# Kernel tuning notes

Hardware: AMD Instinct MI355X
Metric: run time of the kernel (lower is better)

Reference implementation:

```python
import jax, jax.numpy as jnp
import numpy as np

D = 1024  # d_model

def setup_inputs() -> dict:
    key = jax.random.key(0)
    ks = jax.random.split(key, 12)
    s = 1.0 / np.sqrt(D)  # torch Linear default init scale
    inp = {
        "q": jax.random.normal(ks[0], (4, 4096, D), dtype=jnp.float32),
        "k": jax.random.normal(ks[1], (4, 4096, D), dtype=jnp.float32),
        "v": jax.random.normal(ks[2], (4, 4096, D), dtype=jnp.float32),
        "Wq": jax.random.uniform(ks[3], (D, D), jnp.float32, -s, s),
        "bq": jax.random.uniform(ks[4], (D,), jnp.float32, -s, s),
        "Wk": jax.random.uniform(ks[5], (D, D), jnp.float32, -s, s),
        "bk": jax.random.uniform(ks[6], (D,), jnp.float32, -s, s),
        "Wv": jax.random.uniform(ks[7], (D, D), jnp.float32, -s, s),
        "bv": jax.random.uniform(ks[8], (D,), jnp.float32, -s, s),
        "Wo": jax.random.uniform(ks[9], (D, D), jnp.float32, -s, s),
        "bo": jax.random.uniform(ks[10], (D,), jnp.float32, -s, s),
    }
    return inp

def reference(q, k, v, Wq, bq, Wk, bk, Wv, bv, Wo, bo):
    # phi feature map: exp(-x^2 / 2)
    phi = lambda x: jnp.exp(-0.5 * x * x)
    Q = phi(q @ Wq.T + bq)            # [B, N, D]
    K = phi(k @ Wk.T + bk)            # [B, N, D]
    V = v @ Wv.T + bv                 # [B, N, D]
    # linear attention: aggregate K^T V once, then contract with Q
    KV = jnp.einsum('bnd,bnl->bdl', K, V)                 # [B, D, D]
    Z = 1.0 / (jnp.einsum('bnd,bd->bn', Q, K.sum(axis=1)) + 1e-6)  # [B, N]
    out = jnp.einsum('bnd,bdl->bnl', Q, KV) * Z[..., None]         # [B, N, D]
    return out @ Wo.T + bo
```

## Files before the change

kernel.cpp:

```cpp
#include <hip/hip_runtime.h>

typedef unsigned short u16;
typedef unsigned int u32;
typedef unsigned long long u64;

typedef __attribute__((ext_vector_type(8))) short short8;
typedef __attribute__((ext_vector_type(4))) float floatx4;

__device__ __forceinline__ float b2f(u16 h) {
  u32 u = ((u32)h) << 16;
  return __builtin_bit_cast(float, u);
}
__device__ __forceinline__ u16 f2b(float f) {
  u32 u = __builtin_bit_cast(u32, f);
  u32 r = 0x7FFFu + ((u >> 16) & 1u);
  return (u16)((u + r) >> 16);
}

__device__ __forceinline__ void gl_lds16(const void* g, void* l) {
  __builtin_amdgcn_global_load_lds(
      (__attribute__((address_space(1))) void*)(u64)g,
      (__attribute__((address_space(3))) void*)(u32)(u64)l, 16, 0, 0);
}

enum { EPI_PHI_BIAS = 0, EPI_BIAS = 1, EPI_NONE = 2,
       EPI_ZBIAS_F32 = 3 };

template<int EPI, bool TRANS_OUT>
__global__ __launch_bounds__(256)
void gemm_bt(const u16* __restrict__ Ap, const u16* __restrict__ Bp0,
             const float* __restrict__ bias, const float* __restrict__ Zall,
             void* __restrict__ Cp,
             int M, int N, int K, int ldA, int ldB, int ldC,
             long sAb, long sBb, long sCb, long sZb, int abmask, int kshift)
{
  constexpr int BSTRIDE = 16384;
  constexpr int BOFF    = 8192;
  constexpr int SMEM3   = 3 * BSTRIDE;
  constexpr int SMEM    = (TRANS_OUT && 34816 > SMEM3) ? 34816 : SMEM3;
  __shared__ char smem[SMEM];

  const int tid  = threadIdx.x;
  const int lane = tid & 63;
  const int wave = tid >> 6;
  const int wm = wave >> 1, wn = wave & 1;
  const int fl = lane & 15;
  const int q  = lane >> 4;
  const int r4 = q * 4;
  const int bm0 = blockIdx.x * 128, bn0 = blockIdx.y * 128;
  const int bz = blockIdx.z;
  const int abz = bz & abmask;
  const int kbase = (bz >> kshift) * K;

  const u16* Ah = Ap  + (size_t)abz * sAb + kbase;
  const u16* Bh = Bp0 + (size_t)abz * sBb + kbase;

  const u16* gA[2]; const u16* gB[2]; int sL[2];
  #pragma unroll
  for (int n = 0; n < 2; ++n) {
    int j = n * 256 + tid;
    int R = j >> 3, u = (j & 7) ^ (R & 7);
    int r = (R << 1) | (u >> 2), c = u & 3;
    gA[n] = Ah + (size_t)(bm0 + r) * ldA + c * 8;
    gB[n] = Bh + (size_t)(bn0 + r) * ldB + c * 8;
    sL[n] = (n * 256 + wave * 64) * 16;
  }

  int aoff[4], boff[4];
  #pragma unroll
  for (int i = 0; i < 4; ++i) {
    int ra = wm * 64 + i * 16 + fl;
    int Ra = ra >> 1, ua = ((((ra & 1) << 2) | q) ^ (Ra & 7));
    aoff[i] = (Ra * 8 + ua) * 16;
    int rb = wn * 64 + i * 16 + fl;
    int Rb = rb >> 1, ub = ((((rb & 1) << 2) | q) ^ (Rb & 7));
    boff[i] = (Rb * 8 + ub) * 16;
  }

  floatx4 zero = {0.f, 0.f, 0.f, 0.f};
  floatx4 acc[4][4];
  #pragma unroll
  for (int i = 0; i < 4; ++i)
    #pragma unroll
    for (int j = 0; j < 4; ++j) acc[i][j] = zero;

  auto stage = [&](int k0, char* base) {
    #pragma unroll
    for (int n = 0; n < 2; ++n) gl_lds16(gA[n] + k0, base + sL[n]);
    #pragma unroll
    for (int n = 0; n < 2; ++n) gl_lds16(gB[n] + k0, base + BOFF + sL[n]);
  };

  auto kstep = [&](const char* bufc) {
    short8 aF[4], bF[4];
    #pragma unroll
    for (int i = 0; i < 4; ++i) aF[i] = *(const short8*)(bufc + aoff[i]);
    #pragma unroll
    for (int i = 0; i < 4; ++i) bF[i] = *(const short8*)(bufc + BOFF + boff[i]);
    __builtin_amdgcn_s_setprio(1);
    #pragma unroll
    for (int mi = 0; mi < 4; ++mi)
      #pragma unroll
      for (int ni = 0; ni < 4; ++ni)
        acc[mi][ni] = __builtin_amdgcn_mfma_f32_16x16x32_bf16(
            aF[mi], bF[ni], acc[mi][ni], 0, 0, 0);
    __builtin_amdgcn_s_setprio(0);
  };

  const int NIT = K >> 5;
  stage(0, smem);
  stage(32, smem + BSTRIDE);
  asm volatile("s_waitcnt vmcnt(4)\ns_barrier" ::: "memory");
  int c0 = 0, c2 = 2 * BSTRIDE;
  for (int n = 0; n < NIT; ++n) {
    bool pf = n + 2 < NIT;
    if (pf) stage((n + 2) * 32, smem + c2);
    kstep(smem + c0);
    if (n + 1 < NIT) {
      if (pf) asm volatile("s_waitcnt vmcnt(4) lgkmcnt(0)\ns_barrier" ::: "memory");
      else    asm volatile("s_waitcnt vmcnt(0) lgkmcnt(0)\ns_barrier" ::: "memory");
    }
    c0 = c0 == 2 * BSTRIDE ? 0 : c0 + BSTRIDE;
    c2 = c2 == 2 * BSTRIDE ? 0 : c2 + BSTRIDE;
  }

  if constexpr (!TRANS_OUT) {
    #pragma unroll
    for (int mi = 0; mi < 4; ++mi) {
      #pragma unroll
      for (int ni = 0; ni < 4; ++ni) {
        int col = bn0 + wn * 64 + ni * 16 + fl;
        #pragma unroll
        for (int r = 0; r < 4; ++r) {
          int row = bm0 + wm * 64 + mi * 16 + r4 + r;
          float vv = acc[mi][ni][r];
          if constexpr (EPI == EPI_PHI_BIAS) {
            vv += bias[col];
            vv = __expf(-0.5f * vv * vv);
          }
          if constexpr (EPI == EPI_BIAS) vv += bias[col];
          if constexpr (EPI == EPI_ZBIAS_F32)
            vv = vv * Zall[(size_t)abz * sZb + row] + bias[col];
          if constexpr (EPI == EPI_ZBIAS_F32)
            ((float*)Cp)[(size_t)bz * sCb + (size_t)row * ldC + col] = vv;
          else
            ((u16*)Cp)[(size_t)bz * sCb + (size_t)row * ldC + col] = f2b(vv);
        }
      }
    }
  } else {
    __syncthreads();
    u16* sT = (u16*)smem;
    #pragma unroll
    for (int mi = 0; mi < 4; ++mi) {
      #pragma unroll
      for (int ni = 0; ni < 4; ++ni) {
        int colL = wn * 64 + ni * 16 + fl;
        int row0 = wm * 64 + mi * 16 + r4;
        float bcol = bias[bn0 + colL];
        ushort4 h;
        #pragma unroll
        for (int r = 0; r < 4; ++r) {
          float vv = acc[mi][ni][r] + bcol;
          if constexpr (EPI == EPI_PHI_BIAS) vv = __expf(-0.5f * vv * vv);
          ((u16*)&h)[r] = f2b(vv);
        }
        *(ushort4*)(sT + colL * 136 + row0) = h;
      }
    }
    __syncthreads();
    #pragma unroll
    for (int i = 0; i < 8; ++i) {
      int c = tid + i * 256;
      int dloc = c >> 4, t8 = (c & 15) * 8;
      int4 vv = *(const int4*)(sT + dloc * 136 + t8);
      int gd = bn0 + dloc;
      int gt = bm0 + t8;
      int batch = gt >> 12, tt = gt & 4095;
      *(int4*)((u16*)Cp + ((size_t)batch * N + gd) * 4096 + tt) = vv;
    }
  }
}

__global__ __launch_bounds__(256)
void fcvt(const float* __restrict__ src, u16* __restrict__ dst) {
  size_t i = ((size_t)blockIdx.x * 256 + threadIdx.x) * 8;
  float4 a = *(const float4*)(src + i);
  float4 b = *(const float4*)(src + i + 4);
  union { ushort4 h[2]; int4 v; } o;
  o.h[0].x = f2b(a.x); o.h[0].y = f2b(a.y); o.h[0].z = f2b(a.z); o.h[0].w = f2b(a.w);
  o.h[1].x = f2b(b.x); o.h[1].y = f2b(b.y); o.h[1].z = f2b(b.z); o.h[1].w = f2b(b.w);
  *(int4*)(dst + i) = o.v;
}

__global__ __launch_bounds__(256)
void wconv(const float* __restrict__ w0, const float* __restrict__ w1,
           const float* __restrict__ w2, const float* __restrict__ w3,
           u16* __restrict__ dst) {
  unsigned e = blockIdx.x * 256 + threadIdx.x;
  int mat = e >> 18;
  size_t off = (size_t)(e & 262143) * 4;
  const float* src = mat == 0 ? w0 : mat == 1 ? w1 : mat == 2 ? w2 : w3;
  float4 v = *(const float4*)(src + off);
  ushort4 h;
  h.x = f2b(v.x); h.y = f2b(v.y); h.z = f2b(v.z); h.w = f2b(v.w);
  *(ushort4*)(dst + (size_t)mat * 1048576 + off) = h;
}

__global__ __launch_bounds__(256)
void reduce4(const u16* __restrict__ P, u16* __restrict__ out) {
  size_t i = ((size_t)blockIdx.x * 256 + threadIdx.x) * 8;
  int4 a = *(const int4*)(P + i);
  int4 b = *(const int4*)(P + i + 4194304);
  int4 c = *(const int4*)(P + i + 8388608);
  int4 d = *(const int4*)(P + i + 12582912);
  const u16* ha = (const u16*)&a; const u16* hb = (const u16*)&b;
  const u16* hc = (const u16*)&c; const u16* hd = (const u16*)&d;
  ushort4 o0, o1;
  #pragma unroll
  for (int j = 0; j < 8; ++j) {
    float s = b2f(ha[j]) + b2f(hb[j]) + b2f(hc[j]) + b2f(hd[j]);
    ((u16*)(j < 4 ? &o0 : &o1))[j & 3] = f2b(s);
  }
  *(ushort4*)(out + i) = o0;
  *(ushort4*)(out + i + 4) = o1;
}

__global__ __launch_bounds__(256)
void ksum_rows(const u16* __restrict__ KT, float* __restrict__ Ksum) {
  int lane = threadIdx.x & 63;
  int row = blockIdx.x * 4 + (threadIdx.x >> 6);
  const u16* p = KT + (size_t)row * 4096;
  float s = 0.f;
  #pragma unroll
  for (int i = 0; i < 8; ++i) {
    int4 d = *(const int4*)(p + i * 512 + lane * 8);
    const u16* h = (const u16*)&d;
    #pragma unroll
    for (int j = 0; j < 8; ++j) s += b2f(h[j]);
  }
  #pragma unroll
  for (int off = 32; off; off >>= 1) s += __shfl_xor(s, off, 64);
  if (lane == 0) Ksum[row] = s;
}

__global__ __launch_bounds__(256)
void zden(const u16* __restrict__ Qb, const float* __restrict__ Ksum,
          float* __restrict__ Z) {
  int lane = threadIdx.x & 63;
  int t = blockIdx.x * 4 + (threadIdx.x >> 6);
  const u16* qp = Qb + (size_t)t * 1024;
  const float* ks = Ksum + (size_t)(t >> 12) * 1024;
  float s = 0.f;
  #pragma unroll
  for (int i = 0; i < 2; ++i) {
    int idx = i * 512 + lane * 8;
    int4 d = *(const int4*)(qp + idx);
    const u16* h = (const u16*)&d;
    float4 k0 = *(const float4*)(ks + idx);
    float4 k1 = *(const float4*)(ks + idx + 4);
    s += b2f(h[0]) * k0.x + b2f(h[1]) * k0.y + b2f(h[2]) * k0.z + b2f(h[3]) * k0.w
       + b2f(h[4]) * k1.x + b2f(h[5]) * k1.y + b2f(h[6]) * k1.z + b2f(h[7]) * k1.w;
  }
  #pragma unroll
  for (int off = 32; off; off >>= 1) s += __shfl_xor(s, off, 64);
  if (lane == 0) Z[t] = 1.0f / (s + 1e-6f);
}

extern "C" void kernel_launch(void* const* d_in, const int* in_sizes, int n_in,
                              void* d_out, int out_size, void* d_ws, size_t ws_size,
                              hipStream_t stream) {
  const float* q  = (const float*)d_in[0];
  const float* k  = (const float*)d_in[1];
  const float* v  = (const float*)d_in[2];
  const float* Wq = (const float*)d_in[3];
  const float* bq = (const float*)d_in[4];
  const float* Wk = (const float*)d_in[5];
  const float* bk = (const float*)d_in[6];
  const float* Wv = (const float*)d_in[7];
  const float* bv = (const float*)d_in[8];
  const float* Wo = (const float*)d_in[9];
  const float* bo = (const float*)d_in[10];
  float* out = (float*)d_out;

  u16* Wqb = (u16*)d_ws;
  u16* Wkb = Wqb + 1048576;
  u16* Wvb = Wkb + 1048576;
  u16* Wob = Wvb + 1048576;
  u16* Qb  = Wob + 1048576;
  u16* KT  = Qb  + 16777216;
  u16* VT  = KT  + 16777216;
  u16* KVr = VT  + 16777216;
  float* Ksum = (float*)(KVr + 4194304);
  float* Z    = Ksum + 4096;
  u16* kb16 = Qb;
  u16* vb16 = Qb;
  u16* Pkv  = Qb;
  u16* Pg   = VT;
  u16* Gp   = KT;
  u16* qb16 = VT;

  wconv<<<4096, 256, 0, stream>>>(Wq, Wk, Wv, Wo, Wqb);
  fcvt<<<8192, 256, 0, stream>>>(k, kb16);

  dim3 gp(128, 8, 1);
  gemm_bt<EPI_PHI_BIAS, true><<<gp, 256, 0, stream>>>(
      kb16, Wkb, bk, nullptr, KT, 16384, 1024, 1024, 1024, 1024, 0,
      0, 0, 0, 0, 0, 30);
  ksum_rows<<<1024, 256, 0, stream>>>(KT, Ksum);

  fcvt<<<8192, 256, 0, stream>>>(v, vb16);
  gemm_bt<EPI_BIAS, true><<<gp, 256, 0, stream>>>(
      vb16, Wvb, bv, nullptr, VT, 16384, 1024, 1024, 1024, 1024, 0,
      0, 0, 0, 0, 0, 30);

  dim3 g2(8, 8, 16);
  gemm_bt<EPI_NONE, false><<<g2, 256, 0, stream>>>(
      KT, VT, nullptr, nullptr, Pkv, 1024, 1024, 1024, 4096, 4096, 1024,
      4194304L, 4194304L, 1048576L, 0, 3, 2);
  reduce4<<<2048, 256, 0, stream>>>(Pkv, KVr);

  dim3 gg(8, 8, 16);
  gemm_bt<EPI_NONE, false><<<gg, 256, 0, stream>>>(
      Wob, KVr, nullptr, nullptr, Pg, 1024, 1024, 256, 1024, 1024, 1024,
      0L, 1048576L, 1048576L, 0, 3, 2);
  reduce4<<<2048, 256, 0, stream>>>(Pg, Gp);

  fcvt<<<8192, 256, 0, stream>>>(q, qb16);
  gemm_bt<EPI_PHI_BIAS, false><<<gp, 256, 0, stream>>>(
      qb16, Wqb, bq, nullptr, Qb, 16384, 1024, 1024, 1024, 1024, 1024,
      0, 0, 0, 0, 0, 30);
  zden<<<4096, 256, 0, stream>>>(Qb, Ksum, Z);

  dim3 gf(32, 8, 4);
  gemm_bt<EPI_ZBIAS_F32, false><<<gf, 256, 0, stream>>>(
      Qb, Gp, bo, Z, out, 4096, 1024, 1024, 1024, 1024, 1024,
      4194304L, 1048576L, 4194304L, 4096L, 3, 30);
}
```

Before: 342.3 us.

## Add 256x256-tile 512-thread GEMM for projection and output GEMMs

Introduces a gemm_bt256 kernel with 256x256 block tiles, 8 waves each computing a 128x64 sub-tile, and 32 KB per pipeline stage in LDS. It is used for the Q/K/V projections and the final output GEMM, which raises operand reuse per global load and cuts the number of blocks. The transposed-output epilogue now stages through LDS in two halves so the buffer fits. The trade-off is a 96 KB LDS footprint and 128 accumulator registers per thread, which limits occupancy to about one block per CU. The grid also shrinks to roughly one block per CU, which could leave tail imbalance or exposed latency.

```diff
diff --git a/kernel.cpp b/kernel.cpp
--- a/kernel.cpp
+++ b/kernel.cpp
@@ -26,7 +26,7 @@
 enum { EPI_PHI_BIAS = 0, EPI_BIAS = 1, EPI_NONE = 2,
        EPI_ZBIAS_F32 = 3 };
 
-template<int EPI, bool TRANS_OUT>
+template<int EPI>
 __global__ __launch_bounds__(256)
 void gemm_bt(const u16* __restrict__ Ap, const u16* __restrict__ Bp0,
              const float* __restrict__ bias, const float* __restrict__ Zall,
@@ -36,9 +36,7 @@
 {
   constexpr int BSTRIDE = 16384;
   constexpr int BOFF    = 8192;
-  constexpr int SMEM3   = 3 * BSTRIDE;
-  constexpr int SMEM    = (TRANS_OUT && 34816 > SMEM3) ? 34816 : SMEM3;
-  __shared__ char smem[SMEM];
+  __shared__ char smem[3 * BSTRIDE];
 
   const int tid  = threadIdx.x;
   const int lane = tid & 63;
@@ -124,21 +122,138 @@
     c2 = c2 == 2 * BSTRIDE ? 0 : c2 + BSTRIDE;
   }
 
+  #pragma unroll
+  for (int mi = 0; mi < 4; ++mi) {
+    #pragma unroll
+    for (int ni = 0; ni < 4; ++ni) {
+      int col = bn0 + wn * 64 + ni * 16 + fl;
+      #pragma unroll
+      for (int r = 0; r < 4; ++r) {
+        int row = bm0 + wm * 64 + mi * 16 + r4 + r;
+        float vv = acc[mi][ni][r];
+        if constexpr (EPI == EPI_ZBIAS_F32) {
+          vv = vv * Zall[(size_t)abz * sZb + row] + bias[col];
+          ((float*)Cp)[(size_t)bz * sCb + (size_t)row * ldC + col] = vv;
+        } else {
+          ((u16*)Cp)[(size_t)bz * sCb + (size_t)row * ldC + col] = f2b(vv);
+        }
+      }
+    }
+  }
+}
+
+template<int EPI, bool TRANS_OUT>
+__global__ __launch_bounds__(512, 2)
+void gemm_bt256(const u16* __restrict__ Ap, const u16* __restrict__ Bp0,
+                const float* __restrict__ bias, const float* __restrict__ Zall,
+                void* __restrict__ Cp,
+                int M, int N, int K, int ldA, int ldB, int ldC,
+                long sAb, long sBb, long sCb, long sZb, int abmask)
+{
+  constexpr int BSTRIDE = 32768;
+  constexpr int BOFF    = 16384;
+  __shared__ char smem[3 * BSTRIDE];
+
+  const int tid  = threadIdx.x;
+  const int lane = tid & 63;
+  const int wave = tid >> 6;
+  const int wm = wave >> 2, wn = wave & 3;
+  const int fl = lane & 15;
+  const int q  = lane >> 4;
+  const int r4 = q * 4;
+  const int bm0 = blockIdx.x * 256, bn0 = blockIdx.y * 256;
+  const int bz = blockIdx.z;
+  const int abz = bz & abmask;
+
+  const u16* Ah = Ap  + (size_t)abz * sAb;
+  const u16* Bh = Bp0 + (size_t)abz * sBb;
+
+  const u16* gA[2]; const u16* gB[2]; int sL[2];
+  #pragma unroll
+  for (int n = 0; n < 2; ++n) {
+    int j = n * 512 + tid;
+    int R = j >> 3, u = (j & 7) ^ (R & 7);
+    int r = (R << 1) | (u >> 2), c = u & 3;
+    gA[n] = Ah + (size_t)(bm0 + r) * ldA + c * 8;
+    gB[n] = Bh + (size_t)(bn0 + r) * ldB + c * 8;
+    sL[n] = (n * 512 + wave * 64) * 16;
+  }
+
+  int aoff[8], boff[4];
+  #pragma unroll
+  for (int i = 0; i < 8; ++i) {
+    int ra = wm * 128 + i * 16 + fl;
+    int Ra = ra >> 1, ua = ((((ra & 1) << 2) | q) ^ (Ra & 7));
+    aoff[i] = (Ra * 8 + ua) * 16;
+  }
+  #pragma unroll
+  for (int i = 0; i < 4; ++i) {
+    int rb = wn * 64 + i * 16 + fl;
+    int Rb = rb >> 1, ub = ((((rb & 1) << 2) | q) ^ (Rb & 7));
+    boff[i] = (Rb * 8 + ub) * 16;
+  }
+
+  floatx4 zero = {0.f, 0.f, 0.f, 0.f};
+  floatx4 acc[8][4];
+  #pragma unroll
+  for (int i = 0; i < 8; ++i)
+    #pragma unroll
+    for (int j = 0; j < 4; ++j) acc[i][j] = zero;
+
+  auto stage = [&](int k0, char* base) {
+    #pragma unroll
+    for (int n = 0; n < 2; ++n) gl_lds16(gA[n] + k0, base + sL[n]);
+    #pragma unroll
+    for (int n = 0; n < 2; ++n) gl_lds16(gB[n] + k0, base + BOFF + sL[n]);
+  };
+
+  auto kstep = [&](const char* bufc) {
+    short8 bF[4], aF[8];
+    #pragma unroll
+    for (int i = 0; i < 4; ++i) bF[i] = *(const short8*)(bufc + BOFF + boff[i]);
+    #pragma unroll
+    for (int i = 0; i < 8; ++i) aF[i] = *(const short8*)(bufc + aoff[i]);
+    __builtin_amdgcn_s_setprio(1);
+    #pragma unroll
+    for (int mi = 0; mi < 8; ++mi)
+      #pragma unroll
+      for (int ni = 0; ni < 4; ++ni)
+        acc[mi][ni] = __builtin_amdgcn_mfma_f32_16x16x32_bf16(
+            aF[mi], bF[ni], acc[mi][ni], 0, 0, 0);
+    __builtin_amdgcn_s_setprio(0);
+  };
+
+  const int NIT = K >> 5;
+  stage(0, smem);
+  stage(32, smem + BSTRIDE);
+  asm volatile("s_waitcnt vmcnt(4)\ns_barrier" ::: "memory");
+  int c0 = 0, c2 = 2 * BSTRIDE;
+  for (int n = 0; n < NIT; ++n) {
+    bool pf = n + 2 < NIT;
+    if (pf) stage((n + 2) * 32, smem + c2);
+    kstep(smem + c0);
+    if (n + 1 < NIT) {
+      if (pf) asm volatile("s_waitcnt vmcnt(4) lgkmcnt(0)\ns_barrier" ::: "memory");
+      else    asm volatile("s_waitcnt vmcnt(0) lgkmcnt(0)\ns_barrier" ::: "memory");
+    }
+    c0 = c0 == 2 * BSTRIDE ? 0 : c0 + BSTRIDE;
+    c2 = c2 == 2 * BSTRIDE ? 0 : c2 + BSTRIDE;
+  }
+
   if constexpr (!TRANS_OUT) {
     #pragma unroll
-    for (int mi = 0; mi < 4; ++mi) {
+    for (int mi = 0; mi < 8; ++mi) {
       #pragma unroll
       for (int ni = 0; ni < 4; ++ni) {
         int col = bn0 + wn * 64 + ni * 16 + fl;
         #pragma unroll
         for (int r = 0; r < 4; ++r) {
-          int row = bm0 + wm * 64 + mi * 16 + r4 + r;
+          int row = bm0 + wm * 128 + mi * 16 + r4 + r;
           float vv = acc[mi][ni][r];
           if constexpr (EPI == EPI_PHI_BIAS) {
             vv += bias[col];
             vv = __expf(-0.5f * vv * vv);
           }
-          if constexpr (EPI == EPI_BIAS) vv += bias[col];
           if constexpr (EPI == EPI_ZBIAS_F32)
             vv = vv * Zall[(size_t)abz * sZb + row] + bias[col];
           if constexpr (EPI == EPI_ZBIAS_F32)
@@ -149,35 +264,40 @@
       }
     }
   } else {
-    __syncthreads();
     u16* sT = (u16*)smem;
     #pragma unroll
-    for (int mi = 0; mi < 4; ++mi) {
+    for (int p = 0; p < 2; ++p) {
+      __syncthreads();
+      if ((wn >> 1) == p) {
+        #pragma unroll
+        for (int mi = 0; mi < 8; ++mi) {
+          #pragma unroll
+          for (int ni = 0; ni < 4; ++ni) {
+            int colL = wn * 64 + ni * 16 + fl;
+            int row0 = wm * 128 + mi * 16 + r4;
+            float bcol = bias[bn0 + colL];
+            ushort4 h;
+            #pragma unroll
+            for (int r = 0; r < 4; ++r) {
+              float vv = acc[mi][ni][r] + bcol;
+              if constexpr (EPI == EPI_PHI_BIAS) vv = __expf(-0.5f * vv * vv);
+              ((u16*)&h)[r] = f2b(vv);
+            }
+            *(ushort4*)(sT + (colL - p * 128) * 264 + row0) = h;
+          }
+        }
+      }
+      __syncthreads();
       #pragma unroll
-      for (int ni = 0; ni < 4; ++ni) {
-        int colL = wn * 64 + ni * 16 + fl;
-        int row0 = wm * 64 + mi * 16 + r4;
-        float bcol = bias[bn0 + colL];
-        ushort4 h;
-        #pragma unroll
-        for (int r = 0; r < 4; ++r) {
-          float vv = acc[mi][ni][r] + bcol;
-          if constexpr (EPI == EPI_PHI_BIAS) vv = __expf(-0.5f * vv * vv);
-          ((u16*)&h)[r] = f2b(vv);
-        }
-        *(ushort4*)(sT + colL * 136 + row0) = h;
+      for (int i = 0; i < 8; ++i) {
+        int c = tid + i * 512;
+        int dloc = c >> 5, t8 = (c & 31) * 8;
+        int4 vv = *(const int4*)(sT + dloc * 264 + t8);
+        int gd = bn0 + p * 128 + dloc;
+        int gt = bm0 + t8;
+        int batch = gt >> 12, tt = gt & 4095;
+        *(int4*)((u16*)Cp + ((size_t)batch * N + gd) * 4096 + tt) = vv;
       }
-    }
-    __syncthreads();
-    #pragma unroll
-    for (int i = 0; i < 8; ++i) {
-      int c = tid + i * 256;
-      int dloc = c >> 4, t8 = (c & 15) * 8;
-      int4 vv = *(const int4*)(sT + dloc * 136 + t8);
-      int gd = bn0 + dloc;
-      int gt = bm0 + t8;
-      int batch = gt >> 12, tt = gt & 4095;
-      *(int4*)((u16*)Cp + ((size_t)batch * N + gd) * 4096 + tt) = vv;
     }
   }
 }
@@ -303,37 +423,37 @@
   wconv<<<4096, 256, 0, stream>>>(Wq, Wk, Wv, Wo, Wqb);
   fcvt<<<8192, 256, 0, stream>>>(k, kb16);
 
-  dim3 gp(128, 8, 1);
-  gemm_bt<EPI_PHI_BIAS, true><<<gp, 256, 0, stream>>>(
+  dim3 gp(64, 4, 1);
+  gemm_bt256<EPI_PHI_BIAS, true><<<gp, 512, 0, stream>>>(
       kb16, Wkb, bk, nullptr, KT, 16384, 1024, 1024, 1024, 1024, 0,
-      0, 0, 0, 0, 0, 30);
+      0, 0, 0, 0, 0);
   ksum_rows<<<1024, 256, 0, stream>>>(KT, Ksum);
 
   fcvt<<<8192, 256, 0, stream>>>(v, vb16);
-  gemm_bt<EPI_BIAS, true><<<gp, 256, 0, stream>>>(
+  gemm_bt256<EPI_BIAS, true><<<gp, 512, 0, stream>>>(
       vb16, Wvb, bv, nullptr, VT, 16384, 1024, 1024, 1024, 1024, 0,
-      0, 0, 0, 0, 0, 30);
+      0, 0, 0, 0, 0);
 
   dim3 g2(8, 8, 16);
-  gemm_bt<EPI_NONE, false><<<g2, 256, 0, stream>>>(
+  gemm_bt<EPI_NONE><<<g2, 256, 0, stream>>>(
       KT, VT, nullptr, nullptr, Pkv, 1024, 1024, 1024, 4096, 4096, 1024,
       4194304L, 4194304L, 1048576L, 0, 3, 2);
   reduce4<<<2048, 256, 0, stream>>>(Pkv, KVr);
 
   dim3 gg(8, 8, 16);
-  gemm_bt<EPI_NONE, false><<<gg, 256, 0, stream>>>(
+  gemm_bt<EPI_NONE><<<gg, 256, 0, stream>>>(
       Wob, KVr, nullptr, nullptr, Pg, 1024, 1024, 256, 1024, 1024, 1024,
       0L, 1048576L, 1048576L, 0, 3, 2);
   reduce4<<<2048, 256, 0, stream>>>(Pg, Gp);
 
   fcvt<<<8192, 256, 0, stream>>>(q, qb16);
-  gemm_bt<EPI_PHI_BIAS, false><<<gp, 256, 0, stream>>>(
+  gemm_bt256<EPI_PHI_BIAS, false><<<gp, 512, 0, stream>>>(
       qb16, Wqb, bq, nullptr, Qb, 16384, 1024, 1024, 1024, 1024, 1024,
-      0, 0, 0, 0, 0, 30);
+      0, 0, 0, 0, 0);
   zden<<<4096, 256, 0, stream>>>(Qb, Ksum, Z);
 
-  dim3 gf(32, 8, 4);
-  gemm_bt<EPI_ZBIAS_F32, false><<<gf, 256, 0, stream>>>(
+  dim3 gf(16, 4, 4);
+  gemm_bt256<EPI_ZBIAS_F32, false><<<gf, 512, 0, stream>>>(
       Qb, Gp, bo, Z, out, 4096, 1024, 1024, 1024, 1024, 1024,
-      4194304L, 1048576L, 4194304L, 4096L, 3, 30);
-}
+      4194304L, 1048576L, 4194304L, 4096L, 3);
+}
```

Result: faster. 326.4 us (-4.7%).
